# Optimization experiments

Hardware: AMD Instinct MI355X
Metric: run time of the kernel (lower is better)

The kernel has to match this reference:

```python
import jax, jax.numpy as jnp
import numpy as np

B, C, H_IMG, W_IMG = 16, 384, 56, 56
NUM_HEADS = 6
HEAD_DIM = C // NUM_HEADS
BN_EPS = 1e-5


def _bn(x, gamma, beta, mean, var):
    # x: [b, ch, n] or [b, ch, h, w]; per-channel affine normalization (eval-mode BatchNorm)
    shape = (1, -1) + (1,) * (x.ndim - 2)
    scale = (gamma / jnp.sqrt(var + BN_EPS)).reshape(shape)
    shift = (beta - mean * gamma / jnp.sqrt(var + BN_EPS)).reshape(shape)
    return x * scale + shift


def setup_inputs() -> dict:
    key = jax.random.key(0)
    ks = jax.random.split(key, 12)
    c2 = 2 * C
    return {
        "x": jax.random.normal(ks[0], (B, C, H_IMG, W_IMG), jnp.float32),
        "qk_w": jax.random.normal(ks[1], (c2, C // 2), jnp.float32) * 0.05,
        "qk_gamma": jax.random.uniform(ks[2], (c2,), jnp.float32, 0.5, 1.5),
        "qk_beta": jax.random.normal(ks[3], (c2,), jnp.float32) * 0.1,
        "qk_mean": jax.random.normal(ks[4], (c2,), jnp.float32) * 0.1,
        "qk_var": jax.random.uniform(ks[5], (c2,), jnp.float32, 0.5, 1.5),
        "pe_w": jax.random.normal(ks[6], (C, 1, 3, 3), jnp.float32) * 0.1,
        "pe_gamma": jax.random.uniform(ks[7], (C,), jnp.float32, 0.5, 1.5),
        "pe_beta": jax.random.normal(ks[8], (C,), jnp.float32) * 0.1,
        "pe_mean": jax.random.normal(ks[9], (C,), jnp.float32) * 0.1,
        "pe_var": jax.random.uniform(ks[10], (C,), jnp.float32, 0.5, 1.5),
    }


def reference(x, qk_w, qk_gamma, qk_beta, qk_mean, qk_var,
              pe_w, pe_gamma, pe_beta, pe_mean, pe_var):
    b, c, h, w = x.shape
    n = h * w
    s = n ** (-0.5)
    nh, hd = NUM_HEADS, HEAD_DIM

    # grouped (groups=2) 1x1 conv: out channels [0:c] from input [0:c/2], [c:2c] from [c/2:c]
    xg = x.reshape(b, 2, c // 2, n)                       # [b, 2, c/2, n]
    wg = qk_w.reshape(2, c, c // 2)                       # [group, out_per_group, in_per_group]
    qk = jnp.einsum('bgin,goi->bgon', xg, wg).reshape(b, 2 * c, n)
    qk = _bn(qk, qk_gamma, qk_beta, qk_mean, qk_var)
    qk = jax.nn.elu(qk) + 1.0

    qk = qk.reshape(b, 2, nh, hd, n)
    q, k = qk[:, 0], qk[:, 1]                             # [b, H, d, n]
    v = x.reshape(b, nh, hd, n)                           # [b, H, d, n]

    # kv = (k*s) @ (v^T * s): [b, H, d, d]
    kv = jnp.einsum('bhdn,bhen->bhde', k * s, v * s)
    # numerator: q^T @ kv -> [b, H, n, d]
    num = jnp.einsum('bhdn,bhde->bhne', q, kv)
    # denominator: q^T @ mean_n(k) -> [b, H, n]
    den = jnp.einsum('bhdn,bhd->bhn', q, k.mean(axis=-1)) + 1e-6
    attn = (num / den[..., None]).transpose(0, 1, 3, 2).reshape(b, c, h, w)

    # depthwise 3x3 conv positional encoding on v (= x) + BN
    pe = jax.lax.conv_general_dilated(
        x, pe_w, window_strides=(1, 1), padding=((1, 1), (1, 1)),
        feature_group_count=c, dimension_numbers=('NCHW', 'OIHW', 'NCHW'))
    pe = _bn(pe, pe_gamma, pe_beta, pe_mean, pe_var)

    return attn + pe
```

## Files before the change

### kernel.cpp

```cpp
#include <hip/hip_runtime.h>
#include <math.h>

#define N_SP 3136
#define BN_EPS 1e-5f

typedef __attribute__((ext_vector_type(8))) short short8;
typedef __attribute__((ext_vector_type(4))) float f32x4;

#define K_SZ    (16*384*N_SP)
#define QF_OFF  (K_SZ)
#define QF_FSZ  (16*6*49*8192/2)
#define KVP_OFF (QF_OFF + QF_FSZ)
#define KVP_SZ  (16*6*7*64*80)
#define KVT_OFF (KVP_OFF + KVP_SZ)
#define KVT_FSZ (2*96*80*64/2)
#define WH_OFF  (KVT_OFF + KVT_FSZ)
#define WSPLIT_N (2*384*192)

__device__ __forceinline__ void bsplit(float f, ushort& h, ushort& l) {
    uint u = __float_as_uint(f);
    uint hr = (u + 0x7FFFu + ((u >> 16) & 1u)) >> 16;
    h = (ushort)hr;
    float fh = __uint_as_float(hr << 16);
    float fl = f - fh;
    uint v = __float_as_uint(fl);
    l = (ushort)((v + 0x7FFFu + ((v >> 16) & 1u)) >> 16);
}

__global__ __launch_bounds__(256) void p0_wsplit(
    const float* __restrict__ qk_w, ushort* __restrict__ wh, ushort* __restrict__ wl)
{
    int idx = blockIdx.x * 256 + threadIdx.x;
    if (idx >= WSPLIT_N) return;
    ushort h, l;
    bsplit(qk_w[idx], h, l);
    wh[idx] = h;
    wl[idx] = l;
}

__global__ __launch_bounds__(256) void k1_qk_mfma(
    const float* __restrict__ x, const ushort* __restrict__ wh, const ushort* __restrict__ wl,
    const float* __restrict__ gamma, const float* __restrict__ beta,
    const float* __restrict__ mean, const float* __restrict__ var,
    float* __restrict__ k_out, ushort* __restrict__ qf)
{
    __shared__ __align__(16) ushort Ah[8192];
    __shared__ __align__(16) ushort Al[8192];
    __shared__ __align__(16) ushort Bh[4096];
    __shared__ __align__(16) ushort Bl[4096];

    const int bx = blockIdx.x;
    const int bz = blockIdx.y;
    const int by = blockIdx.z;
    const int b = bz >> 1, gg = bz & 1;
    const int t = threadIdx.x;
    const int lane = t & 63, wv = t >> 6;
    const int wr = wv >> 1, wc = wv & 1;
    const int lg = lane >> 4, l15 = lane & 15;

    f32x4 acc[4][2];
    #pragma unroll
    for (int m = 0; m < 4; ++m)
        #pragma unroll
        for (int nf = 0; nf < 2; ++nf)
            acc[m][nf] = (f32x4){0.f, 0.f, 0.f, 0.f};

    const float* xg = x + (size_t)(b * 384 + gg * 192) * N_SP + bx * 64;
    const ushort* whg = wh + (gg * 384 + by * 128) * 192;
    const ushort* wlg = wl + (gg * 384 + by * 128) * 192;

    for (int kt = 0; kt < 3; ++kt) {
        #pragma unroll
        for (int li = 0; li < 4; ++li) {
            int c = li * 256 + t;
            int row = c >> 3, kb = c & 7;
            int goff = row * 192 + kt * 64 + kb * 8;
            float4 vh = *(const float4*)(whg + goff);
            float4 vl = *(const float4*)(wlg + goff);
            int ch = (row * 8 + (kb ^ (row & 7))) * 8;
            *(float4*)&Ah[ch] = vh;
            *(float4*)&Al[ch] = vl;
        }
        #pragma unroll
        for (int li = 0; li < 2; ++li) {
            int idx = li * 256 + t;
            int kp = idx >> 4;
            int nq = idx & 15;
            int k0 = kp * 2;
            const float* px = xg + (size_t)(kt * 64 + k0) * N_SP + nq * 4;
            float4 v0 = *(const float4*)px;
            float4 v1 = *(const float4*)(px + N_SP);
            ushort h0[4], l0[4], h1[4], l1[4];
            float a0[4] = {v0.x, v0.y, v0.z, v0.w};
            float a1[4] = {v1.x, v1.y, v1.z, v1.w};
            #pragma unroll
            for (int i = 0; i < 4; ++i) { bsplit(a0[i], h0[i], l0[i]); bsplit(a1[i], h1[i], l1[i]); }
            int kb = k0 >> 3, ks = (k0 & 6) >> 1;
            #pragma unroll
            for (int i = 0; i < 4; ++i) {
                int n = nq * 4 + i;
                int chunk = n * 8 + (kb ^ ((n >> 1) & 7));
                ((uint*)Bh)[chunk * 4 + ks] = (uint)h0[i] | ((uint)h1[i] << 16);
                ((uint*)Bl)[chunk * 4 + ks] = (uint)l0[i] | ((uint)l1[i] << 16);
            }
        }
        __syncthreads();
        #pragma unroll
        for (int s = 0; s < 2; ++s) {
            short8 ah[4], al[4], bh[2], bl[2];
            int kb = s * 4 + lg;
            #pragma unroll
            for (int m = 0; m < 4; ++m) {
                int row = wr * 64 + m * 16 + l15;
                int ch = (row * 8 + (kb ^ (row & 7))) * 8;
                ah[m] = *(const short8*)&Ah[ch];
                al[m] = *(const short8*)&Al[ch];
            }
            #pragma unroll
            for (int nf = 0; nf < 2; ++nf) {
                int n = wc * 32 + nf * 16 + l15;
                int ch = (n * 8 + (kb ^ ((n >> 1) & 7))) * 8;
                bh[nf] = *(const short8*)&Bh[ch];
                bl[nf] = *(const short8*)&Bl[ch];
            }
            #pragma unroll
            for (int m = 0; m < 4; ++m)
                #pragma unroll
                for (int nf = 0; nf < 2; ++nf) {
                    acc[m][nf] = __builtin_amdgcn_mfma_f32_16x16x32_bf16(ah[m], bh[nf], acc[m][nf], 0, 0, 0);
                    acc[m][nf] = __builtin_amdgcn_mfma_f32_16x16x32_bf16(ah[m], bl[nf], acc[m][nf], 0, 0, 0);
                    acc[m][nf] = __builtin_amdgcn_mfma_f32_16x16x32_bf16(al[m], bh[nf], acc[m][nf], 0, 0, 0);
                }
        }
        __syncthreads();
    }

    float* scs = (float*)Bh;
    float* shs = scs + 128;
    if (t < 128) {
        int ch = gg * 384 + by * 128 + t;
        float sc = gamma[ch] / sqrtf(var[ch] + BN_EPS);
        scs[t] = sc;
        shs[t] = beta[ch] - mean[ch] * sc;
    }
    __syncthreads();

    if (gg == 0) {
        const int head = by * 2 + wr;
        ushort* qbase = qf + ((size_t)(b * 6 + head) * 49 + bx) * 8192;
        #pragma unroll
        for (int m = 0; m < 4; ++m) {
            #pragma unroll
            for (int nf = 0; nf < 2; ++nf) {
                ushort hh[4], ll[4];
                #pragma unroll
                for (int r = 0; r < 4; ++r) {
                    int orow = wr * 64 + m * 16 + lg * 4 + r;
                    float v = acc[m][nf][r] * scs[orow] + shs[orow];
                    v = v > 0.f ? v + 1.f : __expf(v);
                    bsplit(v, hh[r], ll[r]);
                }
                int hc = m * 4 + lg;
                int n = wc * 32 + nf * 16 + l15;
                uint2 uh, ul;
                uh.x = (uint)hh[0] | ((uint)hh[1] << 16);
                uh.y = (uint)hh[2] | ((uint)hh[3] << 16);
                ul.x = (uint)ll[0] | ((uint)ll[1] << 16);
                ul.y = (uint)ll[2] | ((uint)ll[3] << 16);
                *(uint2*)(qbase + (size_t)hc * 256 + n * 4) = uh;
                *(uint2*)(qbase + (size_t)(16 + hc) * 256 + n * 4) = ul;
            }
        }
    } else {
        size_t obase = ((size_t)b * 384 + by * 128) * N_SP + bx * 64 + wc * 32;
        #pragma unroll
        for (int m = 0; m < 4; ++m)
            #pragma unroll
            for (int nf = 0; nf < 2; ++nf) {
                #pragma unroll
                for (int r = 0; r < 4; ++r) {
                    int orow = wr * 64 + m * 16 + lg * 4 + r;
                    float v = acc[m][nf][r] * scs[orow] + shs[orow];
                    v = v > 0.f ? v + 1.f : __expf(v);
                    k_out[obase + (size_t)orow * N_SP + nf * 16 + l15] = v;
                }
            }
    }
}

__global__ __launch_bounds__(256) void k2_kv_mfma(
    const float* __restrict__ x, const float* __restrict__ kbuf,
    float* __restrict__ kv_part)
{
    __shared__ __align__(16) ushort Kh[4096], Kl[4096];
    __shared__ __align__(16) ushort Vh[5120], Vl[5120];

    const int chunk = blockIdx.x;
    const int h = blockIdx.y, b = blockIdx.z;
    const int t = threadIdx.x;
    const int lane = t & 63, wv = t >> 6;
    const int lg = lane >> 4, l15 = lane & 15;

    const float* kp = kbuf + (size_t)(b*384 + h*64) * N_SP;
    const float* vp = x   + (size_t)(b*384 + h*64) * N_SP;

    #pragma unroll
    for (int li = 0; li < 4; ++li) {
        int idx = li * 256 + t;
        int row = 64 + (idx >> 6), col = idx & 63;
        int off = (row * 8 + ((col >> 3) ^ (row & 7))) * 8 + (col & 7);
        Vh[off] = (row == 64) ? (ushort)0x3F80 : (ushort)0;
        Vl[off] = 0;
    }

    f32x4 acc[5];
    #pragma unroll
    for (int nf = 0; nf < 5; ++nf) acc[nf] = (f32x4){0.f, 0.f, 0.f, 0.f};

    for (int sub = 0; sub < 7; ++sub) {
        int n0 = chunk * 448 + sub * 64;
        #pragma unroll
        for (int li = 0; li < 4; ++li) {
            int idx = li * 256 + t;
            int row = idx >> 4, sc = idx & 15;
            int off = (row * 8 + ((sc >> 1) ^ (row & 7))) * 8 + (sc & 1) * 4;
            float4 kf = *(const float4*)&kp[(size_t)row * N_SP + n0 + sc * 4];
            ushort h0,h1,h2,h3,l0,l1,l2,l3;
            bsplit(kf.x,h0,l0); bsplit(kf.y,h1,l1); bsplit(kf.z,h2,l2); bsplit(kf.w,h3,l3);
            ((uint*)&Kh[off])[0] = (uint)h0 | ((uint)h1 << 16);
            ((uint*)&Kh[off])[1] = (uint)h2 | ((uint)h3 << 16);
            ((uint*)&Kl[off])[0] = (uint)l0 | ((uint)l1 << 16);
            ((uint*)&Kl[off])[1] = (uint)l2 | ((uint)l3 << 16);
            float4 vf = *(const float4*)&vp[(size_t)row * N_SP + n0 + sc * 4];
            bsplit(vf.x,h0,l0); bsplit(vf.y,h1,l1); bsplit(vf.z,h2,l2); bsplit(vf.w,h3,l3);
            ((uint*)&Vh[off])[0] = (uint)h0 | ((uint)h1 << 16);
            ((uint*)&Vh[off])[1] = (uint)h2 | ((uint)h3 << 16);
            ((uint*)&Vl[off])[0] = (uint)l0 | ((uint)l1 << 16);
            ((uint*)&Vl[off])[1] = (uint)l2 | ((uint)l3 << 16);
        }
        __syncthreads();
        #pragma unroll
        for (int s = 0; s < 2; ++s) {
            int arow = wv * 16 + l15;
            int akb = (s * 4 + lg) ^ (arow & 7);
            short8 ah = *(const short8*)&Kh[(arow * 8 + akb) * 8];
            short8 al = *(const short8*)&Kl[(arow * 8 + akb) * 8];
            #pragma unroll
            for (int nf = 0; nf < 5; ++nf) {
                int brow = nf * 16 + l15;
                int bkb = (s * 4 + lg) ^ (brow & 7);
                short8 bh = *(const short8*)&Vh[(brow * 8 + bkb) * 8];
                short8 bl = *(const short8*)&Vl[(brow * 8 + bkb) * 8];
                acc[nf] = __builtin_amdgcn_mfma_f32_16x16x32_bf16(ah, bh, acc[nf], 0, 0, 0);
                acc[nf] = __builtin_amdgcn_mfma_f32_16x16x32_bf16(ah, bl, acc[nf], 0, 0, 0);
                acc[nf] = __builtin_amdgcn_mfma_f32_16x16x32_bf16(al, bh, acc[nf], 0, 0, 0);
            }
        }
        __syncthreads();
    }

    size_t base = (size_t)((b*6 + h)*7 + chunk) * 64 * 80;
    #pragma unroll
    for (int nf = 0; nf < 5; ++nf)
        #pragma unroll
        for (int r = 0; r < 4; ++r) {
            int d = wv * 16 + lg * 4 + r;
            kv_part[base + (size_t)d * 80 + nf * 16 + l15] = acc[nf][r];
        }
}

__global__ __launch_bounds__(256) void k2b_reduce(
    const float* __restrict__ kv_part,
    ushort* __restrict__ kvt_h, ushort* __restrict__ kvt_l)
{
    const int bh = blockIdx.x;
    const int t = threadIdx.x;
    const float inv_n = 1.0f / (float)N_SP;
    const float* base = kv_part + (size_t)bh * 7 * 5120;
    ushort* oh = kvt_h + (size_t)bh * 5120;
    ushort* ol = kvt_l + (size_t)bh * 5120;
    float s[20];
    #pragma unroll
    for (int j = 0; j < 20; ++j) s[j] = 0.f;
    for (int c = 0; c < 7; ++c) {
        #pragma unroll
        for (int j = 0; j < 20; ++j) s[j] += base[c * 5120 + j * 256 + t];
    }
    #pragma unroll
    for (int j = 0; j < 20; ++j) {
        int i = j * 256 + t;
        int d = i / 80, e = i % 80;
        ushort h, l;
        bsplit(s[j] * inv_n, h, l);
        oh[e * 64 + d] = h;
        ol[e * 64 + d] = l;
    }
}

__device__ __forceinline__ void load_qfrag(const ushort* qtile, int wv, int lg, int l15,
                                           short8* qh, short8* ql)
{
    #pragma unroll
    for (int s = 0; s < 2; ++s) {
        int hc = (s * 4 + lg) * 2;
        const ushort* ph = qtile + hc * 256 + (wv * 16 + l15) * 4;
        uint2 a0 = *(const uint2*)ph;
        uint2 a1 = *(const uint2*)(ph + 256);
        uint* bh = (uint*)&qh[s];
        bh[0] = a0.x; bh[1] = a0.y; bh[2] = a1.x; bh[3] = a1.y;
        const ushort* pl = ph + 16 * 256;
        uint2 c0 = *(const uint2*)pl;
        uint2 c1 = *(const uint2*)(pl + 256);
        uint* bl = (uint*)&ql[s];
        bl[0] = c0.x; bl[1] = c0.y; bl[2] = c1.x; bl[3] = c1.y;
    }
}

#define ATT_STRIDE 68
__global__ __launch_bounds__(256) void k3a_attn(
    const ushort* __restrict__ qf,
    const ushort* __restrict__ kvt_h, const ushort* __restrict__ kvt_l,
    float* __restrict__ out)
{
    __shared__ __align__(16) float SBF[ATT_STRIDE * 64 + 64];

    const int bx = blockIdx.x;
    const int h = blockIdx.y, b = blockIdx.z;
    const int t = threadIdx.x;
    const int lane = t & 63, wv = t >> 6;
    const int lg = lane >> 4, l15 = lane & 15;
    const int n0 = bx * 64;

    const ushort* qtile = qf + ((size_t)(b * 6 + h) * 49 + bx) * 8192;
    short8 bqh[2], bql[2];
    load_qfrag(qtile, wv, lg, l15, bqh, bql);

    const ushort* ahb = kvt_h + (size_t)(b * 6 + h) * 5120;
    const ushort* alb = kvt_l + (size_t)(b * 6 + h) * 5120;
    f32x4 acc[5];
    #pragma unroll
    for (int m = 0; m < 5; ++m) acc[m] = (f32x4){0.f, 0.f, 0.f, 0.f};
    #pragma unroll
    for (int s = 0; s < 2; ++s) {
        #pragma unroll
        for (int m = 0; m < 5; ++m) {
            int off = (m * 16 + l15) * 64 + (s * 4 + lg) * 8;
            short8 ah = *(const short8*)&ahb[off];
            short8 al = *(const short8*)&alb[off];
            acc[m] = __builtin_amdgcn_mfma_f32_16x16x32_bf16(ah, bqh[s], acc[m], 0, 0, 0);
            acc[m] = __builtin_amdgcn_mfma_f32_16x16x32_bf16(ah, bql[s], acc[m], 0, 0, 0);
            acc[m] = __builtin_amdgcn_mfma_f32_16x16x32_bf16(al, bqh[s], acc[m], 0, 0, 0);
        }
    }

    {
        int ncol = wv * 16 + l15;
        #pragma unroll
        for (int m = 0; m < 4; ++m)
            #pragma unroll
            for (int r = 0; r < 4; ++r)
                SBF[(m * 16 + lg * 4 + r) * ATT_STRIDE + ncol] = acc[m][r];
        if (lg == 0)
            SBF[ATT_STRIDE * 64 + ncol] = acc[4][0];
    }
    __syncthreads();

    const int tx = t & 15, ty = t >> 4;
    const int p0 = n0 + tx * 4;
    float den[4];
    #pragma unroll
    for (int p = 0; p < 4; ++p) den[p] = SBF[ATT_STRIDE * 64 + tx * 4 + p] + 1e-6f;
    #pragma unroll
    for (int j = 0; j < 4; ++j) {
        int cc = ty * 4 + j;
        int c = h * 64 + cc;
        float4 r;
        float* pr = (float*)&r;
        #pragma unroll
        for (int p = 0; p < 4; ++p)
            pr[p] = SBF[cc * ATT_STRIDE + tx * 4 + p] / den[p];
        *(float4*)&out[((size_t)b * 384 + c) * N_SP + p0] = r;
    }
}

__global__ __launch_bounds__(256) void k3b_pe(
    const float* __restrict__ x, const float* __restrict__ pw,
    const float* __restrict__ pgamma, const float* __restrict__ pbeta,
    const float* __restrict__ pmean, const float* __restrict__ pvar,
    float* __restrict__ out)
{
    const int bc = blockIdx.x;
    const int c = bc & 383;
    const int cc = bc % 384;
    (void)c;
    const float* xp = x + (size_t)bc * N_SP;
    float* op = out + (size_t)bc * N_SP;
    float w9[9];
    #pragma unroll
    for (int q = 0; q < 9; ++q) w9[q] = pw[cc * 9 + q];
    float sc = pgamma[cc] / sqrtf(pvar[cc] + BN_EPS);
    float sh = pbeta[cc] - pmean[cc] * sc;

    for (int s = threadIdx.x; s < 392; s += 256) {
        int y = s / 7, xs = (s % 7) * 8;
        float row[3][10];
        #pragma unroll
        for (int dy = 0; dy < 3; ++dy) {
            int yy = y + dy - 1;
            bool yok = (yy >= 0) && (yy < 56);
            if (yok) {
                const float* xr = xp + yy * 56;
                float4 a = *(const float4*)&xr[xs];
                float4 bq = *(const float4*)&xr[xs + 4];
                row[dy][1] = a.x;  row[dy][2] = a.y;  row[dy][3] = a.z;  row[dy][4] = a.w;
                row[dy][5] = bq.x; row[dy][6] = bq.y; row[dy][7] = bq.z; row[dy][8] = bq.w;
                row[dy][0] = (xs > 0)  ? xr[xs - 1] : 0.f;
                row[dy][9] = (xs < 48) ? xr[xs + 8] : 0.f;
            } else {
                #pragma unroll
                for (int i = 0; i < 10; ++i) row[dy][i] = 0.f;
            }
        }
        float* po = op + y * 56 + xs;
        float4 o0 = *(const float4*)po;
        float4 o1 = *(const float4*)(po + 4);
        float ov[8] = {o0.x, o0.y, o0.z, o0.w, o1.x, o1.y, o1.z, o1.w};
        #pragma unroll
        for (int p = 0; p < 8; ++p) {
            float conv = 0.f;
            #pragma unroll
            for (int dy = 0; dy < 3; ++dy)
                #pragma unroll
                for (int dx = 0; dx < 3; ++dx)
                    conv += w9[dy * 3 + dx] * row[dy][p + dx];
            ov[p] += conv * sc + sh;
        }
        float4 r0 = make_float4(ov[0], ov[1], ov[2], ov[3]);
        float4 r1 = make_float4(ov[4], ov[5], ov[6], ov[7]);
        *(float4*)po = r0;
        *(float4*)(po + 4) = r1;
    }
}

extern "C" void kernel_launch(void* const* d_in, const int* in_sizes, int n_in,
                              void* d_out, int out_size, void* d_ws, size_t ws_size,
                              hipStream_t stream)
{
    const float* x        = (const float*)d_in[0];
    const float* qk_w     = (const float*)d_in[1];
    const float* qk_gamma = (const float*)d_in[2];
    const float* qk_beta  = (const float*)d_in[3];
    const float* qk_mean  = (const float*)d_in[4];
    const float* qk_var   = (const float*)d_in[5];
    const float* pe_w     = (const float*)d_in[6];
    const float* pe_gamma = (const float*)d_in[7];
    const float* pe_beta  = (const float*)d_in[8];
    const float* pe_mean  = (const float*)d_in[9];
    const float* pe_var   = (const float*)d_in[10];
    float* out = (float*)d_out;

    float* ws      = (float*)d_ws;
    float* kbuf    = ws;
    ushort* qf     = (ushort*)(ws + QF_OFF);
    float* kv_part = ws + KVP_OFF;
    ushort* kvt_h  = (ushort*)(ws + KVT_OFF);
    ushort* kvt_l  = kvt_h + 96 * 5120;
    ushort* whp    = (ushort*)(ws + WH_OFF);
    ushort* wlp    = whp + WSPLIT_N;

    hipLaunchKernelGGL(p0_wsplit, dim3((WSPLIT_N + 255)/256), dim3(256), 0, stream,
                       qk_w, whp, wlp);
    dim3 g1(49, 32, 3);
    hipLaunchKernelGGL(k1_qk_mfma, g1, dim3(256), 0, stream,
                       x, whp, wlp, qk_gamma, qk_beta, qk_mean, qk_var, kbuf, qf);
    dim3 g2(7, 6, 16);
    hipLaunchKernelGGL(k2_kv_mfma, g2, dim3(256), 0, stream, x, kbuf, kv_part);
    hipLaunchKernelGGL(k2b_reduce, dim3(96), dim3(256), 0, stream,
                       kv_part, kvt_h, kvt_l);
    dim3 g3(49, 6, 16);
    hipLaunchKernelGGL(k3a_attn, g3, dim3(256), 0, stream,
                       qf, kvt_h, kvt_l, out);
    hipLaunchKernelGGL(k3b_pe, dim3(6144), dim3(256), 0, stream,
                       x, pe_w, pe_gamma, pe_beta, pe_mean, pe_var, out);
}
```

Before: 238.8 us.

## Move PE conv first, pre-split K to bf16 pairs, reorder k1 grid and swizzle

The depthwise PE conv now runs first and writes out directly. The attention kernel reads that value and adds it, so the later read-modify-write pass over out is gone. k1 now stores K as packed bf16 hi/lo pairs, which lets k2 skip re-splitting K. k1's grid order is swapped so the channel-tile index varies faster, probably for better x reuse in cache, and the B-tile LDS swizzle is changed to cut bank conflicts. The PE pass now reads x early, while out is read once in k3a.

```diff
diff --git a/kernel.cpp b/kernel.cpp
--- a/kernel.cpp
+++ b/kernel.cpp
@@ -17,6 +17,8 @@
 #define WH_OFF  (KVT_OFF + KVT_FSZ)
 #define WSPLIT_N (2*384*192)
 
+#define FSWZ(n) ((((n) >> 1) ^ ((n) >> 2)) & 7)
+
 __device__ __forceinline__ void bsplit(float f, ushort& h, ushort& l) {
     uint u = __float_as_uint(f);
     uint hr = (u + 0x7FFFu + ((u >> 16) & 1u)) >> 16;
@@ -38,11 +40,64 @@
     wl[idx] = l;
 }
 
+__global__ __launch_bounds__(256) void k0_pe(
+    const float* __restrict__ x, const float* __restrict__ pw,
+    const float* __restrict__ pgamma, const float* __restrict__ pbeta,
+    const float* __restrict__ pmean, const float* __restrict__ pvar,
+    float* __restrict__ out)
+{
+    const int bc = blockIdx.x;
+    const int cc = bc % 384;
+    const float* xp = x + (size_t)bc * N_SP;
+    float* op = out + (size_t)bc * N_SP;
+    float w9[9];
+    #pragma unroll
+    for (int q = 0; q < 9; ++q) w9[q] = pw[cc * 9 + q];
+    float sc = pgamma[cc] / sqrtf(pvar[cc] + BN_EPS);
+    float sh = pbeta[cc] - pmean[cc] * sc;
+
+    for (int s = threadIdx.x; s < 392; s += 256) {
+        int y = s / 7, xs = (s % 7) * 8;
+        float row[3][10];
+        #pragma unroll
+        for (int dy = 0; dy < 3; ++dy) {
+            int yy = y + dy - 1;
+            bool yok = (yy >= 0) && (yy < 56);
+            if (yok) {
+                const float* xr = xp + yy * 56;
+                float4 a = *(const float4*)&xr[xs];
+                float4 bq = *(const float4*)&xr[xs + 4];
+                row[dy][1] = a.x;  row[dy][2] = a.y;  row[dy][3] = a.z;  row[dy][4] = a.w;
+                row[dy][5] = bq.x; row[dy][6] = bq.y; row[dy][7] = bq.z; row[dy][8] = bq.w;
+                row[dy][0] = (xs > 0)  ? xr[xs - 1] : 0.f;
+                row[dy][9] = (xs < 48) ? xr[xs + 8] : 0.f;
+            } else {
+                #pragma unroll
+                for (int i = 0; i < 10; ++i) row[dy][i] = 0.f;
+            }
+        }
+        float ov[8];
+        #pragma unroll
+        for (int p = 0; p < 8; ++p) {
+            float conv = 0.f;
+            #pragma unroll
+            for (int dy = 0; dy < 3; ++dy)
+                #pragma unroll
+                for (int dx = 0; dx < 3; ++dx)
+                    conv += w9[dy * 3 + dx] * row[dy][p + dx];
+            ov[p] = conv * sc + sh;
+        }
+        float* po = op + y * 56 + xs;
+        *(float4*)po = make_float4(ov[0], ov[1], ov[2], ov[3]);
+        *(float4*)(po + 4) = make_float4(ov[4], ov[5], ov[6], ov[7]);
+    }
+}
+
 __global__ __launch_bounds__(256) void k1_qk_mfma(
     const float* __restrict__ x, const ushort* __restrict__ wh, const ushort* __restrict__ wl,
     const float* __restrict__ gamma, const float* __restrict__ beta,
     const float* __restrict__ mean, const float* __restrict__ var,
-    float* __restrict__ k_out, ushort* __restrict__ qf)
+    uint* __restrict__ kq, ushort* __restrict__ qf)
 {
     __shared__ __align__(16) ushort Ah[8192];
     __shared__ __align__(16) ushort Al[8192];
@@ -50,8 +105,8 @@
     __shared__ __align__(16) ushort Bl[4096];
 
     const int bx = blockIdx.x;
-    const int bz = blockIdx.y;
-    const int by = blockIdx.z;
+    const int by = blockIdx.y;
+    const int bz = blockIdx.z;
     const int b = bz >> 1, gg = bz & 1;
     const int t = threadIdx.x;
     const int lane = t & 63, wv = t >> 6;
@@ -99,7 +154,7 @@
             #pragma unroll
             for (int i = 0; i < 4; ++i) {
                 int n = nq * 4 + i;
-                int chunk = n * 8 + (kb ^ ((n >> 1) & 7));
+                int chunk = n * 8 + (kb ^ FSWZ(n));
                 ((uint*)Bh)[chunk * 4 + ks] = (uint)h0[i] | ((uint)h1[i] << 16);
                 ((uint*)Bl)[chunk * 4 + ks] = (uint)l0[i] | ((uint)l1[i] << 16);
             }
@@ -119,7 +174,7 @@
             #pragma unroll
             for (int nf = 0; nf < 2; ++nf) {
                 int n = wc * 32 + nf * 16 + l15;
-                int ch = (n * 8 + (kb ^ ((n >> 1) & 7))) * 8;
+                int ch = (n * 8 + (kb ^ FSWZ(n))) * 8;
                 bh[nf] = *(const short8*)&Bh[ch];
                 bl[nf] = *(const short8*)&Bl[ch];
             }
@@ -182,14 +237,16 @@
                     int orow = wr * 64 + m * 16 + lg * 4 + r;
                     float v = acc[m][nf][r] * scs[orow] + shs[orow];
                     v = v > 0.f ? v + 1.f : __expf(v);
-                    k_out[obase + (size_t)orow * N_SP + nf * 16 + l15] = v;
+                    ushort hh, ll;
+                    bsplit(v, hh, ll);
+                    kq[obase + (size_t)orow * N_SP + nf * 16 + l15] = (uint)hh | ((uint)ll << 16);
                 }
             }
     }
 }
 
 __global__ __launch_bounds__(256) void k2_kv_mfma(
-    const float* __restrict__ x, const float* __restrict__ kbuf,
+    const float* __restrict__ x, const uint* __restrict__ kq,
     float* __restrict__ kv_part)
 {
     __shared__ __align__(16) ushort Kh[4096], Kl[4096];
@@ -201,8 +258,8 @@
     const int lane = t & 63, wv = t >> 6;
     const int lg = lane >> 4, l15 = lane & 15;
 
-    const float* kp = kbuf + (size_t)(b*384 + h*64) * N_SP;
-    const float* vp = x   + (size_t)(b*384 + h*64) * N_SP;
+    const uint* kp  = kq + (size_t)(b*384 + h*64) * N_SP;
+    const float* vp = x  + (size_t)(b*384 + h*64) * N_SP;
 
     #pragma unroll
     for (int li = 0; li < 4; ++li) {
@@ -224,14 +281,13 @@
             int idx = li * 256 + t;
             int row = idx >> 4, sc = idx & 15;
             int off = (row * 8 + ((sc >> 1) ^ (row & 7))) * 8 + (sc & 1) * 4;
-            float4 kf = *(const float4*)&kp[(size_t)row * N_SP + n0 + sc * 4];
+            uint4 kf = *(const uint4*)&kp[(size_t)row * N_SP + n0 + sc * 4];
+            ((uint*)&Kh[off])[0] = (kf.x & 0xFFFFu) | (kf.y << 16);
+            ((uint*)&Kh[off])[1] = (kf.z & 0xFFFFu) | (kf.w << 16);
+            ((uint*)&Kl[off])[0] = (kf.x >> 16) | (kf.y & 0xFFFF0000u);
+            ((uint*)&Kl[off])[1] = (kf.z >> 16) | (kf.w & 0xFFFF0000u);
+            float4 vf = *(const float4*)&vp[(size_t)row * N_SP + n0 + sc * 4];
             ushort h0,h1,h2,h3,l0,l1,l2,l3;
-            bsplit(kf.x,h0,l0); bsplit(kf.y,h1,l1); bsplit(kf.z,h2,l2); bsplit(kf.w,h3,l3);
-            ((uint*)&Kh[off])[0] = (uint)h0 | ((uint)h1 << 16);
-            ((uint*)&Kh[off])[1] = (uint)h2 | ((uint)h3 << 16);
-            ((uint*)&Kl[off])[0] = (uint)l0 | ((uint)l1 << 16);
-            ((uint*)&Kl[off])[1] = (uint)l2 | ((uint)l3 << 16);
-            float4 vf = *(const float4*)&vp[(size_t)row * N_SP + n0 + sc * 4];
             bsplit(vf.x,h0,l0); bsplit(vf.y,h1,l1); bsplit(vf.z,h2,l2); bsplit(vf.w,h3,l3);
             ((uint*)&Vh[off])[0] = (uint)h0 | ((uint)h1 << 16);
             ((uint*)&Vh[off])[1] = (uint)h2 | ((uint)h3 << 16);
@@ -374,71 +430,15 @@
     for (int j = 0; j < 4; ++j) {
         int cc = ty * 4 + j;
         int c = h * 64 + cc;
+        float* po = &out[((size_t)b * 384 + c) * N_SP + p0];
+        float4 pe = *(const float4*)po;
+        const float* pep = (const float*)&pe;
         float4 r;
         float* pr = (float*)&r;
         #pragma unroll
         for (int p = 0; p < 4; ++p)
-            pr[p] = SBF[cc * ATT_STRIDE + tx * 4 + p] / den[p];
-        *(float4*)&out[((size_t)b * 384 + c) * N_SP + p0] = r;
-    }
-}
-
-__global__ __launch_bounds__(256) void k3b_pe(
-    const float* __restrict__ x, const float* __restrict__ pw,
-    const float* __restrict__ pgamma, const float* __restrict__ pbeta,
-    const float* __restrict__ pmean, const float* __restrict__ pvar,
-    float* __restrict__ out)
-{
-    const int bc = blockIdx.x;
-    const int c = bc & 383;
-    const int cc = bc % 384;
-    (void)c;
-    const float* xp = x + (size_t)bc * N_SP;
-    float* op = out + (size_t)bc * N_SP;
-    float w9[9];
-    #pragma unroll
-    for (int q = 0; q < 9; ++q) w9[q] = pw[cc * 9 + q];
-    float sc = pgamma[cc] / sqrtf(pvar[cc] + BN_EPS);
-    float sh = pbeta[cc] - pmean[cc] * sc;
-
-    for (int s = threadIdx.x; s < 392; s += 256) {
-        int y = s / 7, xs = (s % 7) * 8;
-        float row[3][10];
-        #pragma unroll
-        for (int dy = 0; dy < 3; ++dy) {
-            int yy = y + dy - 1;
-            bool yok = (yy >= 0) && (yy < 56);
-            if (yok) {
-                const float* xr = xp + yy * 56;
-                float4 a = *(const float4*)&xr[xs];
-                float4 bq = *(const float4*)&xr[xs + 4];
-                row[dy][1] = a.x;  row[dy][2] = a.y;  row[dy][3] = a.z;  row[dy][4] = a.w;
-                row[dy][5] = bq.x; row[dy][6] = bq.y; row[dy][7] = bq.z; row[dy][8] = bq.w;
-                row[dy][0] = (xs > 0)  ? xr[xs - 1] : 0.f;
-                row[dy][9] = (xs < 48) ? xr[xs + 8] : 0.f;
-            } else {
-                #pragma unroll
-                for (int i = 0; i < 10; ++i) row[dy][i] = 0.f;
-            }
-        }
-        float* po = op + y * 56 + xs;
-        float4 o0 = *(const float4*)po;
-        float4 o1 = *(const float4*)(po + 4);
-        float ov[8] = {o0.x, o0.y, o0.z, o0.w, o1.x, o1.y, o1.z, o1.w};
-        #pragma unroll
-        for (int p = 0; p < 8; ++p) {
-            float conv = 0.f;
-            #pragma unroll
-            for (int dy = 0; dy < 3; ++dy)
-                #pragma unroll
-                for (int dx = 0; dx < 3; ++dx)
-                    conv += w9[dy * 3 + dx] * row[dy][p + dx];
-            ov[p] += conv * sc + sh;
-        }
-        float4 r0 = make_float4(ov[0], ov[1], ov[2], ov[3]);
-        float4 r1 = make_float4(ov[4], ov[5], ov[6], ov[7]);
-        *(float4*)po = r0;
-        *(float4*)(po + 4) = r1;
+            pr[p] = SBF[cc * ATT_STRIDE + tx * 4 + p] / den[p] + pep[p];
+        *(float4*)po = r;
     }
 }
 
@@ -460,7 +460,7 @@
     float* out = (float*)d_out;
 
     float* ws      = (float*)d_ws;
-    float* kbuf    = ws;
+    uint* kq       = (uint*)ws;
     ushort* qf     = (ushort*)(ws + QF_OFF);
     float* kv_part = ws + KVP_OFF;
     ushort* kvt_h  = (ushort*)(ws + KVT_OFF);
@@ -470,16 +470,16 @@
 
     hipLaunchKernelGGL(p0_wsplit, dim3((WSPLIT_N + 255)/256), dim3(256), 0, stream,
                        qk_w, whp, wlp);
-    dim3 g1(49, 32, 3);
+    hipLaunchKernelGGL(k0_pe, dim3(6144), dim3(256), 0, stream,
+                       x, pe_w, pe_gamma, pe_beta, pe_mean, pe_var, out);
+    dim3 g1(49, 3, 32);
     hipLaunchKernelGGL(k1_qk_mfma, g1, dim3(256), 0, stream,
-                       x, whp, wlp, qk_gamma, qk_beta, qk_mean, qk_var, kbuf, qf);
+                       x, whp, wlp, qk_gamma, qk_beta, qk_mean, qk_var, kq, qf);
     dim3 g2(7, 6, 16);
-    hipLaunchKernelGGL(k2_kv_mfma, g2, dim3(256), 0, stream, x, kbuf, kv_part);
+    hipLaunchKernelGGL(k2_kv_mfma, g2, dim3(256), 0, stream, x, kq, kv_part);
     hipLaunchKernelGGL(k2b_reduce, dim3(96), dim3(256), 0, stream,
                        kv_part, kvt_h, kvt_l);
     dim3 g3(49, 6, 16);
     hipLaunchKernelGGL(k3a_attn, g3, dim3(256), 0, stream,
                        qf, kvt_h, kvt_l, out);
-    hipLaunchKernelGGL(k3b_pe, dim3(6144), dim3(256), 0, stream,
-                       x, pe_w, pe_gamma, pe_beta, pe_mean, pe_var, out);
-}
+}
```

Measured after the change: 242.8 us. About the same (+1.7%).
